# Kernel optimization log

Measured on AMD Instinct MI355X. Metric: run time of the kernel, lower is better.

Reference implementation:

```python
import jax, jax.numpy as jnp
import numpy as np

N_NODES = 100000
D = 40


def sgconv(x, src, dst, W, b, n_nodes):
    """PyG SGConv with K=1: symmetric gcn_norm with self-loops, then linear."""
    # add self loops
    loop = jnp.arange(n_nodes, dtype=src.dtype)
    s = jnp.concatenate([src, loop])
    d = jnp.concatenate([dst, loop])
    ones = jnp.ones(s.shape[0], dtype=x.dtype)
    deg = jax.ops.segment_sum(ones, d, num_segments=n_nodes)
    dinv = jnp.where(deg > 0, jax.lax.rsqrt(deg), 0.0)
    norm = dinv[s] * dinv[d]                      # [E+N]
    msg = norm[:, None] * x[s]                    # gather + scale, [E+N, D]
    agg = jax.ops.segment_sum(msg, d, num_segments=n_nodes)  # scatter-add, [N, D]
    return agg @ W.T + b


def setup_inputs() -> dict:
    key = jax.random.key(0)
    k1, k2, k3, k4, k5, k6 = jax.random.split(key, 6)
    x = jax.random.normal(k1, (N_NODES, D), dtype=jnp.float32)
    edge_index = jax.random.randint(k2, (2, 1600000), 0, N_NODES, dtype=jnp.int64)
    s = 1.0 / np.sqrt(D)
    W1 = jax.random.uniform(k3, (D, D), jnp.float32, -s, s)
    b1 = jax.random.uniform(k4, (D,), jnp.float32, -s, s)
    W2 = jax.random.uniform(k5, (D, D), jnp.float32, -s, s)
    b2 = jax.random.uniform(k6, (D,), jnp.float32, -s, s)
    return {"x": x, "edge_index": edge_index, "W1": W1, "b1": b1, "W2": W2, "b2": b2}


def reference(x, edge_index, W1, b1, W2, b2):
    src, dst = edge_index[0], edge_index[1]
    n = x.shape[0]
    h = jax.nn.relu(sgconv(x, src, dst, W1, b1, n))
    out = sgconv(h, src, dst, W2, b2, n)
    return out.reshape(n * out.shape[1])  # generalizes x.view(1600)
```

## Files before the change

### kernel.cpp

```cpp
#include <hip/hip_runtime.h>
#include <hip/hip_fp16.h>

#define DD 40
#define PITER 8
#define NP 512
#define SROW_LD 44
#define SWT_LD 41

__global__ void k_binA(const int* __restrict__ src, const int* __restrict__ dst,
                       int* __restrict__ gcur, unsigned* __restrict__ ebin,
                       int E, int PS, unsigned M, int CAPB) {
  __shared__ int hist[NP];
  __shared__ int curs[NP];
  const int tid = threadIdx.x;
  hist[tid] = 0;
  hist[tid + 256] = 0;
  __syncthreads();
  const int base = blockIdx.x * (256 * PITER);
  for (int it = 0; it < PITER; ++it) {
    int i = base + it * 256 + tid;
    if (i < E) {
      unsigned t = (unsigned)dst[i];
      int b = (int)(((unsigned long long)t * M) >> 31);
      atomicAdd(&hist[b], 1);
    }
  }
  __syncthreads();
#pragma unroll
  for (int q = 0; q < 2; ++q) {
    int b = tid + q * 256;
    int h = hist[b];
    int old = h ? atomicAdd(&gcur[b], h) : 0;
    curs[b] = b * CAPB + old;
  }
  __syncthreads();
  for (int it = 0; it < PITER; ++it) {
    int i = base + it * 256 + tid;
    if (i < E) {
      unsigned t = (unsigned)dst[i];
      int b = (int)(((unsigned long long)t * M) >> 31);
      unsigned local = t - (unsigned)(b * PS);
      int pos = atomicAdd(&curs[b], 1);
      ebin[pos] = (local << 17) | (unsigned)src[i];
    }
  }
}

__global__ __launch_bounds__(256) void k_partB(
    const unsigned* __restrict__ ebin, const int* __restrict__ gcur,
    int* __restrict__ ideg, int* __restrict__ cursor, float* __restrict__ dinv,
    int* __restrict__ es, int* __restrict__ nodeord,
    int PS, int CAPB, int CAPE, int n) {
  __shared__ int sdeg[256];
  __shared__ int sbuf[2][256];
  __shared__ int scur[256];
  __shared__ int dh[64];
  const int p = blockIdx.x;
  const int tid = threadIdx.x;
  const int start = p * CAPB;
  const int cnt = gcur[p];

  sdeg[tid] = 0;
  if (tid < 64) dh[tid] = 0;
  if (tid < PS) nodeord[p * PS + tid] = -1;
  __syncthreads();
  for (int i = tid; i < cnt; i += 256) atomicAdd(&sdeg[ebin[start + i] >> 17], 1);
  __syncthreads();

  int v = sdeg[tid];
  sbuf[0][tid] = v;
  __syncthreads();
  int pi = 0;
  for (int off = 1; off < 256; off <<= 1) {
    int x = sbuf[pi][tid];
    if (tid >= off) x += sbuf[pi][tid - off];
    sbuf[pi ^ 1][tid] = x;
    __syncthreads();
    pi ^= 1;
  }
  int incl = sbuf[pi][tid];
  scur[tid] = incl - v;

  const int node = p * PS + tid;
  const int isnode = (tid < PS && node < n);
  const int dc = min(v, 63);
  if (isnode) {
    ideg[node] = v;
    cursor[node] = p * CAPE + incl;
    dinv[node] = rsqrtf((float)(v + 1));
    atomicAdd(&dh[dc], 1);
  }
  __syncthreads();

  if (tid == 0) {
    int s = 0;
    for (int q = 0; q < 64; ++q) { int h = dh[q]; dh[q] = s; s += h; }
  }
  __syncthreads();
  if (isnode) {
    int r = atomicAdd(&dh[dc], 1);
    nodeord[p * PS + r] = node;
  }

  for (int i = tid; i < cnt; i += 256) {
    unsigned pk = ebin[start + i];
    int l = (int)(pk >> 17);
    int pos = atomicAdd(&scur[l], 1);
    es[p * CAPE + pos] = (int)(pk & 0x1FFFFu);
  }
}

__global__ void k_prescale(const float4* __restrict__ x4, const float* __restrict__ dinv,
                           uint2* __restrict__ xs8, int n4) {
  int i = blockIdx.x * blockDim.x + threadIdx.x;
  if (i < n4) {
    float w = dinv[i / 10];
    float4 v = x4[i];
    __half2 ha = __float22half2_rn(make_float2(v.x * w, v.y * w));
    __half2 hb = __float22half2_rn(make_float2(v.z * w, v.w * w));
    uint2 u;
    u.x = *(unsigned*)&ha;
    u.y = *(unsigned*)&hb;
    xs8[i] = u;
  }
}

template <int OUT_HALF>
__global__ __launch_bounds__(256) void k_layer(
    const uint4* __restrict__ in4, const int* __restrict__ es,
    const int* __restrict__ ideg, const int* __restrict__ cursor,
    const float* __restrict__ dinv, const int* __restrict__ nodeord,
    const float* __restrict__ W, const float* __restrict__ bias,
    float* __restrict__ outf, __half2* __restrict__ outh, int nslots) {
  __shared__ float sWT[DD * SWT_LD];
  __shared__ float sb[DD];
  __shared__ float srow[48][SROW_LD];
  __shared__ int svnode[48];
  const int tid = threadIdx.x;

  if (tid < 48) {
    int slot = blockIdx.x * 48 + tid;
    svnode[tid] = (slot < nslots) ? nodeord[slot] : -1;
  }
  __syncthreads();

  const int w = tid >> 6, lane = tid & 63;
  const int g = lane / 5, pos = lane - g * 5;
  const int v = (g < 12) ? svnode[w * 12 + g] : -1;

#define ACC8(U, A)                                   \
  {                                                  \
    const __half2* hh = (const __half2*)&(U);        \
    float2 f0 = __half22float2(hh[0]);               \
    float2 f1 = __half22float2(hh[1]);               \
    float2 f2 = __half22float2(hh[2]);               \
    float2 f3 = __half22float2(hh[3]);               \
    A[0] += f0.x; A[1] += f0.y; A[2] += f1.x;        \
    A[3] += f1.y; A[4] += f2.x; A[5] += f2.y;        \
    A[6] += f3.x; A[7] += f3.y;                      \
  }

  if (v >= 0) {
    const int e1 = cursor[v];
    int e = e1 - ideg[v];
    float a[8], b[8];
    {
      uint4 u = in4[(size_t)v * 5 + pos];
      const __half2* hh = (const __half2*)&u;
      float2 f0 = __half22float2(hh[0]);
      float2 f1 = __half22float2(hh[1]);
      float2 f2 = __half22float2(hh[2]);
      float2 f3 = __half22float2(hh[3]);
      a[0] = f0.x; a[1] = f0.y; a[2] = f1.x; a[3] = f1.y;
      a[4] = f2.x; a[5] = f2.y; a[6] = f3.x; a[7] = f3.y;
#pragma unroll
      for (int q = 0; q < 8; ++q) b[q] = 0.f;
    }
    int n0, n1, n2, n3, n4, n5, n6, n7;
    bool have = (e + 7 < e1);
    if (have) {
      n0 = es[e];     n1 = es[e + 1]; n2 = es[e + 2]; n3 = es[e + 3];
      n4 = es[e + 4]; n5 = es[e + 5]; n6 = es[e + 6]; n7 = es[e + 7];
    }
    while (have) {
      int s0 = n0, s1 = n1, s2 = n2, s3 = n3, s4 = n4, s5 = n5, s6 = n6, s7 = n7;
      int en = e + 8;
      have = (en + 7 < e1);
      if (have) {
        n0 = es[en];     n1 = es[en + 1]; n2 = es[en + 2]; n3 = es[en + 3];
        n4 = es[en + 4]; n5 = es[en + 5]; n6 = es[en + 6]; n7 = es[en + 7];
      }
      uint4 u0 = in4[(size_t)s0 * 5 + pos];
      uint4 u1 = in4[(size_t)s1 * 5 + pos];
      uint4 u2 = in4[(size_t)s2 * 5 + pos];
      uint4 u3 = in4[(size_t)s3 * 5 + pos];
      uint4 u4 = in4[(size_t)s4 * 5 + pos];
      uint4 u5 = in4[(size_t)s5 * 5 + pos];
      uint4 u6 = in4[(size_t)s6 * 5 + pos];
      uint4 u7 = in4[(size_t)s7 * 5 + pos];
      ACC8(u0, a); ACC8(u1, b); ACC8(u2, a); ACC8(u3, b);
      ACC8(u4, a); ACC8(u5, b); ACC8(u6, a); ACC8(u7, b);
      e = en;
    }
    for (; e + 3 < e1; e += 4) {
      int s0 = es[e], s1 = es[e + 1], s2 = es[e + 2], s3 = es[e + 3];
      uint4 u0 = in4[(size_t)s0 * 5 + pos];
      uint4 u1 = in4[(size_t)s1 * 5 + pos];
      uint4 u2 = in4[(size_t)s2 * 5 + pos];
      uint4 u3 = in4[(size_t)s3 * 5 + pos];
      ACC8(u0, a); ACC8(u1, b); ACC8(u2, a); ACC8(u3, b);
    }
    for (; e < e1; ++e) {
      uint4 uu = in4[(size_t)es[e] * 5 + pos];
      ACC8(uu, a);
    }
    float* r = &srow[w * 12 + g][pos * 8];
#pragma unroll
    for (int q = 0; q < 8; ++q) r[q] = a[q] + b[q];
  }

  for (int t = tid; t < DD * DD; t += 256) sWT[(t % DD) * SWT_LD + t / DD] = W[t];
  if (tid < DD) sb[tid] = bias[tid];
  __syncthreads();

  if (OUT_HALF) {
    for (int i = tid; i < 48 * 20; i += 256) {
      int l = i / 20, jj = i - l * 20;
      int vv = svnode[l];
      if (vv >= 0) {
        float dv = dinv[vv];
        const float* row = srow[l];
        float s0 = 0.f, s1 = 0.f;
#pragma unroll
        for (int k = 0; k < DD; ++k) {
          s0 = fmaf(row[k], sWT[k * SWT_LD + 2 * jj], s0);
          s1 = fmaf(row[k], sWT[k * SWT_LD + 2 * jj + 1], s1);
        }
        s0 = fmaf(s0, dv, sb[2 * jj]);
        s1 = fmaf(s1, dv, sb[2 * jj + 1]);
        s0 = fmaxf(s0, 0.f) * dv;
        s1 = fmaxf(s1, 0.f) * dv;
        outh[(size_t)vv * 20 + jj] = __float22half2_rn(make_float2(s0, s1));
      }
    }
  } else {
    for (int i = tid; i < 48 * DD; i += 256) {
      int l = i / DD, j = i - l * DD;
      int vv = svnode[l];
      if (vv >= 0) {
        float dv = dinv[vv];
        const float* row = srow[l];
        float acc = 0.f;
#pragma unroll
        for (int k = 0; k < DD; ++k) acc = fmaf(row[k], sWT[k * SWT_LD + j], acc);
        outf[(size_t)vv * DD + j] = fmaf(acc, dv, sb[j]);
      }
    }
  }
#undef ACC8
}

extern "C" void kernel_launch(void* const* d_in, const int* in_sizes, int n_in,
                              void* d_out, int out_size, void* d_ws, size_t ws_size,
                              hipStream_t stream) {
  const float* x = (const float*)d_in[0];
  const int* ei = (const int*)d_in[1];
  const float* W1 = (const float*)d_in[2];
  const float* b1 = (const float*)d_in[3];
  const float* W2 = (const float*)d_in[4];
  const float* b2 = (const float*)d_in[5];

  const int n = in_sizes[0] / DD;
  const int E = in_sizes[1] / 2;
  const int* src = ei;
  const int* dst = ei + E;
  const int n4 = n * (DD / 4);
  const int PS = (n + NP - 1) / NP;
  const unsigned M = (unsigned)((((unsigned long long)1 << 31) + PS - 1) / PS);
  const int CAPB = E / NP + 512;
  const int CAPE = CAPB;
  const int NCH = (E + 256 * PITER - 1) / (256 * PITER);
  const int NSLOT = NP * PS;

  float* out = (float*)d_out;

  char* w = (char*)d_ws;
  float* dinv = (float*)w;   w += (size_t)n * 4;
  int* ideg = (int*)w;       w += (size_t)n * 4;
  int* cursor = (int*)w;     w += (size_t)n * 4;
  int* gcur = (int*)w;       w += (size_t)NP * 4;
  int* nodeord = (int*)w;    w += (size_t)NSLOT * 4;
  char* ebin_hs = w;         w += (size_t)n * DD * 2;
  int* es = (int*)w;         w += (size_t)NP * CAPE * 4;
  uint2* xs8 = (uint2*)w;    w += (size_t)n * DD * 2;

  unsigned* ebin = (unsigned*)ebin_hs;
  uint2* hs8 = (uint2*)ebin_hs;

  hipMemsetAsync(gcur, 0, (size_t)NP * 4, stream);

  k_binA<<<NCH, 256, 0, stream>>>(src, dst, gcur, ebin, E, PS, M, CAPB);
  k_partB<<<NP, 256, 0, stream>>>(ebin, gcur, ideg, cursor, dinv, es, nodeord,
                                  PS, CAPB, CAPE, n);
  k_prescale<<<(n4 + 255) / 256, 256, 0, stream>>>((const float4*)x, dinv, xs8, n4);

  const int NBK = (NSLOT + 47) / 48;
  k_layer<1><<<NBK, 256, 0, stream>>>((const uint4*)xs8, es, ideg, cursor, dinv, nodeord,
                                      W1, b1, nullptr, (__half2*)hs8, NSLOT);
  k_layer<0><<<NBK, 256, 0, stream>>>((const uint4*)hs8, es, ideg, cursor, dinv, nodeord,
                                      W2, b2, out, nullptr, NSLOT);
}
```

Baseline: 162.1 us.

## Sort edges in shared memory before binning, fuse prescale into partition kernel

The binning kernel now processes 8K edges per block and first sorts them by bin in shared memory, so the global writes to each bin's window come out contiguous instead of scattered. Global bin counters are padded to avoid false sharing. The partition size is fixed at 192 nodes per bin with 521 bins. The per-bin node ordering now ranks nodes by degree within each 48-node window using a direct count, replacing the atomic histogram. The x prescale-to-half kernel is folded into the partition kernel, which removes one launch but hardcodes PS=192 and NP=521, so it is tied to n near 100000.

```diff
diff --git a/kernel.cpp b/kernel.cpp
--- a/kernel.cpp
+++ b/kernel.cpp
@@ -2,73 +2,47 @@
 #include <hip/hip_fp16.h>
 
 #define DD 40
-#define PITER 8
-#define NP 512
+#define PITER 32
+#define NP 521
+#define NPAD 544
+#define PS 192
 #define SROW_LD 44
 #define SWT_LD 41
-
-__global__ void k_binA(const int* __restrict__ src, const int* __restrict__ dst,
-                       int* __restrict__ gcur, unsigned* __restrict__ ebin,
-                       int E, int PS, unsigned M, int CAPB) {
-  __shared__ int hist[NP];
-  __shared__ int curs[NP];
+#define GC_PAD 16
+#define BAE (256 * PITER)
+#define ALIGN16(x) (((x) + 15) & ~(size_t)15)
+
+__global__ __launch_bounds__(256) void k_binA(
+    const int* __restrict__ src, const int* __restrict__ dst,
+    int* __restrict__ gcur, unsigned* __restrict__ ebin,
+    int E, unsigned M, int CAPB) {
+  __shared__ unsigned ssort[BAE];
+  __shared__ int sdest[BAE];
+  __shared__ int hist[NPAD];
+  __shared__ int binstart[NPAD];
+  __shared__ int curs[NPAD];
+  __shared__ int win[NPAD];
+  __shared__ int sbuf[2][256];
   const int tid = threadIdx.x;
-  hist[tid] = 0;
-  hist[tid + 256] = 0;
-  __syncthreads();
-  const int base = blockIdx.x * (256 * PITER);
+  const int base = blockIdx.x * BAE;
+  const int cnt = min(BAE, E - base);
+
+  for (int b = tid; b < NPAD; b += 256) hist[b] = 0;
+  __syncthreads();
   for (int it = 0; it < PITER; ++it) {
-    int i = base + it * 256 + tid;
-    if (i < E) {
-      unsigned t = (unsigned)dst[i];
+    int i = it * 256 + tid;
+    if (i < cnt) {
+      unsigned t = (unsigned)dst[base + i];
       int b = (int)(((unsigned long long)t * M) >> 31);
       atomicAdd(&hist[b], 1);
     }
   }
   __syncthreads();
-#pragma unroll
-  for (int q = 0; q < 2; ++q) {
-    int b = tid + q * 256;
-    int h = hist[b];
-    int old = h ? atomicAdd(&gcur[b], h) : 0;
-    curs[b] = b * CAPB + old;
-  }
-  __syncthreads();
-  for (int it = 0; it < PITER; ++it) {
-    int i = base + it * 256 + tid;
-    if (i < E) {
-      unsigned t = (unsigned)dst[i];
-      int b = (int)(((unsigned long long)t * M) >> 31);
-      unsigned local = t - (unsigned)(b * PS);
-      int pos = atomicAdd(&curs[b], 1);
-      ebin[pos] = (local << 17) | (unsigned)src[i];
-    }
-  }
-}
-
-__global__ __launch_bounds__(256) void k_partB(
-    const unsigned* __restrict__ ebin, const int* __restrict__ gcur,
-    int* __restrict__ ideg, int* __restrict__ cursor, float* __restrict__ dinv,
-    int* __restrict__ es, int* __restrict__ nodeord,
-    int PS, int CAPB, int CAPE, int n) {
-  __shared__ int sdeg[256];
-  __shared__ int sbuf[2][256];
-  __shared__ int scur[256];
-  __shared__ int dh[64];
-  const int p = blockIdx.x;
-  const int tid = threadIdx.x;
-  const int start = p * CAPB;
-  const int cnt = gcur[p];
-
-  sdeg[tid] = 0;
-  if (tid < 64) dh[tid] = 0;
-  if (tid < PS) nodeord[p * PS + tid] = -1;
-  __syncthreads();
-  for (int i = tid; i < cnt; i += 256) atomicAdd(&sdeg[ebin[start + i] >> 17], 1);
-  __syncthreads();
-
-  int v = sdeg[tid];
-  sbuf[0][tid] = v;
+  int b0 = 3 * tid, b1 = 3 * tid + 1, b2 = 3 * tid + 2;
+  int h0 = (b0 < NPAD) ? hist[b0] : 0;
+  int h1 = (b1 < NPAD) ? hist[b1] : 0;
+  int h2 = (b2 < NPAD) ? hist[b2] : 0;
+  sbuf[0][tid] = h0 + h1 + h2;
   __syncthreads();
   int pi = 0;
   for (int off = 1; off < 256; off <<= 1) {
@@ -78,50 +52,107 @@
     __syncthreads();
     pi ^= 1;
   }
+  int excl = sbuf[pi][tid] - (h0 + h1 + h2);
+  if (b0 < NPAD) { binstart[b0] = excl;            curs[b0] = excl; }
+  if (b1 < NPAD) { binstart[b1] = excl + h0;       curs[b1] = excl + h0; }
+  if (b2 < NPAD) { binstart[b2] = excl + h0 + h1;  curs[b2] = excl + h0 + h1; }
+  for (int b = tid; b < NPAD; b += 256) {
+    int h = hist[b];
+    win[b] = h ? (b * CAPB + atomicAdd(&gcur[b * GC_PAD], h)) : 0;
+  }
+  __syncthreads();
+  for (int it = 0; it < PITER; ++it) {
+    int i = it * 256 + tid;
+    if (i < cnt) {
+      unsigned t = (unsigned)dst[base + i];
+      int b = (int)(((unsigned long long)t * M) >> 31);
+      unsigned local = t - (unsigned)(b * PS);
+      int pos = atomicAdd(&curs[b], 1);
+      ssort[pos] = (local << 17) | (unsigned)src[base + i];
+      sdest[pos] = win[b] + (pos - binstart[b]);
+    }
+  }
+  __syncthreads();
+  for (int k = tid; k < cnt; k += 256) ebin[sdest[k]] = ssort[k];
+}
+
+__global__ __launch_bounds__(256) void k_partB(
+    const unsigned* __restrict__ ebin, const int* __restrict__ gcur,
+    const float4* __restrict__ x4,
+    int* __restrict__ ideg, int* __restrict__ cursor, float* __restrict__ dinv,
+    int* __restrict__ es, int* __restrict__ nodeord, uint2* __restrict__ xs8,
+    int CAPB, int CAPE, int n) {
+  __shared__ int sdeg[256];
+  __shared__ int sbuf[2][256];
+  __shared__ int scur[256];
+  __shared__ float sdv[PS];
+  const int p = blockIdx.x;
+  const int tid = threadIdx.x;
+  const int start = p * CAPB;
+  const int cnt = gcur[p * GC_PAD];
+
+  sdeg[tid] = 0;
+  if (tid < PS) nodeord[p * PS + tid] = -1;
+  __syncthreads();
+  for (int i = tid; i < cnt; i += 256)
+    atomicAdd(&sdeg[(ebin[start + i] >> 17) & 0xFF], 1);
+  __syncthreads();
+
+  int v = sdeg[tid];
+  sbuf[0][tid] = v;
+  __syncthreads();
+  int pi = 0;
+  for (int off = 1; off < 256; off <<= 1) {
+    int x = sbuf[pi][tid];
+    if (tid >= off) x += sbuf[pi][tid - off];
+    sbuf[pi ^ 1][tid] = x;
+    __syncthreads();
+    pi ^= 1;
+  }
   int incl = sbuf[pi][tid];
   scur[tid] = incl - v;
 
   const int node = p * PS + tid;
-  const int isnode = (tid < PS && node < n);
-  const int dc = min(v, 63);
+  const bool isnode = (tid < PS && node < n);
   if (isnode) {
     ideg[node] = v;
     cursor[node] = p * CAPE + incl;
-    dinv[node] = rsqrtf((float)(v + 1));
-    atomicAdd(&dh[dc], 1);
-  }
-  __syncthreads();
-
-  if (tid == 0) {
-    int s = 0;
-    for (int q = 0; q < 64; ++q) { int h = dh[q]; dh[q] = s; s += h; }
-  }
-  __syncthreads();
-  if (isnode) {
-    int r = atomicAdd(&dh[dc], 1);
-    nodeord[p * PS + r] = node;
+    float dv = rsqrtf((float)(v + 1));
+    dinv[node] = dv;
+    sdv[tid] = dv;
+  }
+  __syncthreads();
+
+  if (tid < PS) {
+    int wstart = (tid / 48) * 48;
+    int rank = 0;
+    for (int j = 0; j < 48; ++j) {
+      int dj = sdeg[wstart + j];
+      rank += (dj < v) || (dj == v && (wstart + j) < tid);
+    }
+    if (isnode) nodeord[p * PS + wstart + rank] = node;
   }
 
   for (int i = tid; i < cnt; i += 256) {
     unsigned pk = ebin[start + i];
-    int l = (int)(pk >> 17);
+    int l = (int)((pk >> 17) & 0xFF);
     int pos = atomicAdd(&scur[l], 1);
     es[p * CAPE + pos] = (int)(pk & 0x1FFFFu);
   }
-}
-
-__global__ void k_prescale(const float4* __restrict__ x4, const float* __restrict__ dinv,
-                           uint2* __restrict__ xs8, int n4) {
-  int i = blockIdx.x * blockDim.x + threadIdx.x;
-  if (i < n4) {
-    float w = dinv[i / 10];
-    float4 v = x4[i];
-    __half2 ha = __float22half2_rn(make_float2(v.x * w, v.y * w));
-    __half2 hb = __float22half2_rn(make_float2(v.z * w, v.w * w));
-    uint2 u;
-    u.x = *(unsigned*)&ha;
-    u.y = *(unsigned*)&hb;
-    xs8[i] = u;
+
+  for (int i = tid; i < PS * 10; i += 256) {
+    int l = i / 10, part = i - l * 10;
+    int gn = p * PS + l;
+    if (gn < n) {
+      float w = sdv[l];
+      float4 vv = x4[(size_t)gn * 10 + part];
+      __half2 ha = __float22half2_rn(make_float2(vv.x * w, vv.y * w));
+      __half2 hb = __float22half2_rn(make_float2(vv.z * w, vv.w * w));
+      uint2 u;
+      u.x = *(unsigned*)&ha;
+      u.y = *(unsigned*)&hb;
+      xs8[(size_t)gn * 10 + part] = u;
+    }
   }
 }
 
@@ -274,37 +305,34 @@
   const int E = in_sizes[1] / 2;
   const int* src = ei;
   const int* dst = ei + E;
-  const int n4 = n * (DD / 4);
-  const int PS = (n + NP - 1) / NP;
   const unsigned M = (unsigned)((((unsigned long long)1 << 31) + PS - 1) / PS);
   const int CAPB = E / NP + 512;
   const int CAPE = CAPB;
-  const int NCH = (E + 256 * PITER - 1) / (256 * PITER);
+  const int NCH = (E + BAE - 1) / BAE;
   const int NSLOT = NP * PS;
 
   float* out = (float*)d_out;
 
   char* w = (char*)d_ws;
-  float* dinv = (float*)w;   w += (size_t)n * 4;
-  int* ideg = (int*)w;       w += (size_t)n * 4;
-  int* cursor = (int*)w;     w += (size_t)n * 4;
-  int* gcur = (int*)w;       w += (size_t)NP * 4;
-  int* nodeord = (int*)w;    w += (size_t)NSLOT * 4;
-  char* ebin_hs = w;         w += (size_t)n * DD * 2;
-  int* es = (int*)w;         w += (size_t)NP * CAPE * 4;
-  uint2* xs8 = (uint2*)w;    w += (size_t)n * DD * 2;
+  float* dinv = (float*)w;   w += ALIGN16((size_t)n * 4);
+  int* ideg = (int*)w;       w += ALIGN16((size_t)n * 4);
+  int* cursor = (int*)w;     w += ALIGN16((size_t)n * 4);
+  int* gcur = (int*)w;       w += ALIGN16((size_t)NPAD * GC_PAD * 4);
+  int* nodeord = (int*)w;    w += ALIGN16((size_t)NSLOT * 4);
+  char* ebin_hs = w;         w += ALIGN16((size_t)n * 80);
+  int* es = (int*)w;         w += ALIGN16((size_t)NP * CAPE * 4);
+  uint2* xs8 = (uint2*)w;    w += ALIGN16((size_t)n * 80);
 
   unsigned* ebin = (unsigned*)ebin_hs;
   uint2* hs8 = (uint2*)ebin_hs;
 
-  hipMemsetAsync(gcur, 0, (size_t)NP * 4, stream);
-
-  k_binA<<<NCH, 256, 0, stream>>>(src, dst, gcur, ebin, E, PS, M, CAPB);
-  k_partB<<<NP, 256, 0, stream>>>(ebin, gcur, ideg, cursor, dinv, es, nodeord,
-                                  PS, CAPB, CAPE, n);
-  k_prescale<<<(n4 + 255) / 256, 256, 0, stream>>>((const float4*)x, dinv, xs8, n4);
-
-  const int NBK = (NSLOT + 47) / 48;
+  hipMemsetAsync(gcur, 0, (size_t)NPAD * GC_PAD * 4, stream);
+
+  k_binA<<<NCH, 256, 0, stream>>>(src, dst, gcur, ebin, E, M, CAPB);
+  k_partB<<<NP, 256, 0, stream>>>(ebin, gcur, (const float4*)x, ideg, cursor, dinv,
+                                  es, nodeord, xs8, CAPB, CAPE, n);
+
+  const int NBK = NSLOT / 48;
   k_layer<1><<<NBK, 256, 0, stream>>>((const uint4*)xs8, es, ideg, cursor, dinv, nodeord,
                                       W1, b1, nullptr, (__half2*)hs8, NSLOT);
   k_layer<0><<<NBK, 256, 0, stream>>>((const uint4*)hs8, es, ideg, cursor, dinv, nodeord,
```

New measurement: 160.5 us. No clear change (-1.0%).
